# Kernel tuning notes

Measured on AMD Instinct MI355X. Metric: run time of the kernel, lower is better.

The kernel has to match this reference:

```python
import jax, jax.numpy as jnp
import numpy as np

N_GAUSS = 2048
FEAT_DIM = 3
IMG_H, IMG_W = 256, 256
EPS = 1e-4  # args.eps with tiled rasterizer path


def setup_inputs() -> dict:
    key = jax.random.key(0)
    k_xy, k_sc, k_rot, k_feat = jax.random.split(key, 4)
    xy = jax.random.uniform(k_xy, (N_GAUSS, 2), dtype=jnp.float32)  # normalized [0,1) coords
    # scale holds INVERSE std-devs (disable_inverse_scale=False path: scale = 1/init_scale);
    # values 10..50 give Gaussians spanning a few pixels at 256x256.
    scale = jax.random.uniform(k_sc, (N_GAUSS, 2), minval=10.0, maxval=50.0, dtype=jnp.float32)
    rot = jax.random.normal(k_rot, (N_GAUSS, 1), dtype=jnp.float32)
    feat = jax.random.uniform(k_feat, (N_GAUSS, FEAT_DIM), dtype=jnp.float32)
    return {"xy": xy, "scale": scale, "rot": rot, "feat": feat, "topk": 8}


def reference(xy, scale, rot, feat, topk):
    # Pixel centers in normalized coordinates, matching get_grid(h, w) -> (x, y)
    xs = (jnp.arange(IMG_W, dtype=jnp.float32) + 0.5) / IMG_W
    ys = (jnp.arange(IMG_H, dtype=jnp.float32) + 0.5) / IMG_H
    px, py = jnp.meshgrid(xs, ys, indexing="xy")  # each [H, W]
    px = px.reshape(-1)  # [P]
    py = py.reshape(-1)

    dx = px[:, None] - xy[None, :, 0]  # [P, N]
    dy = py[:, None] - xy[None, :, 1]  # [P, N]

    c = jnp.cos(rot[:, 0])  # [N]
    s = jnp.sin(rot[:, 0])
    # Rotate offset into the Gaussian's local frame
    lx = dx * c + dy * s   # [P, N]
    ly = -dx * s + dy * c  # [P, N]

    # Anisotropic Gaussian weight; scale is the inverse std-dev per axis
    w = jnp.exp(-0.5 * ((lx * scale[:, 0]) ** 2 + (ly * scale[:, 1]) ** 2))  # [P, N]

    # Keep top-k Gaussians per pixel, normalize their weights, accumulate features
    tw, ti = jax.lax.top_k(w, topk)        # [P, K]
    tf = feat[ti]                          # [P, K, C]
    alpha = tw / (jnp.sum(tw, axis=-1, keepdims=True) + EPS)  # [P, K]
    img = jnp.einsum("pk,pkc->pc", alpha, tf)                 # [P, C]
    return img.reshape(IMG_H, IMG_W, FEAT_DIM).transpose(2, 0, 1)  # [C, H, W]
```

## Files before the change

### kernel.cpp

```cpp
#include <hip/hip_runtime.h>
#include <math.h>

#define N_GAUSS 2048
#define IMG_H 256
#define IMG_W 256
#define NPIX (IMG_H * IMG_W)
#define EPS 1e-4f

#define TILE 8
#define TILES_X (IMG_W / TILE)
#define NTILES (TILES_X * (IMG_H / TILE))
#define SEG 512
#define SEGCAP 128
#define D_HALF 0.019336f

#define LADDER(T, G)                                                     \
    if ((T) < v7) {                                                      \
        const bool c0 = (T) < v0, c1 = (T) < v1, c2 = (T) < v2;          \
        const bool c3 = (T) < v3, c4 = (T) < v4, c5 = (T) < v5;          \
        const bool c6 = (T) < v6;                                        \
        v7 = c6 ? v6 : (T);            i7 = c6 ? i6 : (G);               \
        v6 = c6 ? (c5 ? v5 : (T)) : v6; i6 = c6 ? (c5 ? i5 : (G)) : i6;  \
        v5 = c5 ? (c4 ? v4 : (T)) : v5; i5 = c5 ? (c4 ? i4 : (G)) : i5;  \
        v4 = c4 ? (c3 ? v3 : (T)) : v4; i4 = c4 ? (c3 ? i3 : (G)) : i4;  \
        v3 = c3 ? (c2 ? v2 : (T)) : v3; i3 = c3 ? (c2 ? i2 : (G)) : i3;  \
        v2 = c2 ? (c1 ? v1 : (T)) : v2; i2 = c2 ? (c1 ? i1 : (G)) : i2;  \
        v1 = c1 ? (c0 ? v0 : (T)) : v1; i1 = c1 ? (c0 ? i0 : (G)) : i1;  \
        v0 = c0 ? (T) : v0;            i0 = c0 ? (G) : i0;               \
    }

#define CE(a, i, j)                                   \
    { float lo_ = fminf(a[i], a[j]);                  \
      float hi_ = fmaxf(a[i], a[j]);                  \
      a[i] = lo_; a[j] = hi_; }

#define SORT8(a)                                      \
    CE(a,0,1) CE(a,2,3) CE(a,4,5) CE(a,6,7)           \
    CE(a,0,2) CE(a,1,3) CE(a,4,6) CE(a,5,7)           \
    CE(a,1,2) CE(a,5,6)                               \
    CE(a,0,4) CE(a,1,5) CE(a,2,6) CE(a,3,7)           \
    CE(a,2,4) CE(a,3,5)                               \
    CE(a,1,2) CE(a,3,4) CE(a,5,6)

__device__ __forceinline__ void top8_butterfly(float (&cur)[8]) {
#pragma unroll
    for (int m = 1; m < 64; m <<= 1) {
        float oth[8];
#pragma unroll
        for (int k = 0; k < 8; ++k) oth[k] = __shfl_xor(cur[k], m, 64);
        float t_[8];
#pragma unroll
        for (int k = 0; k < 8; ++k) t_[k] = fminf(cur[k], oth[7 - k]);
        CE(t_,0,4) CE(t_,1,5) CE(t_,2,6) CE(t_,3,7)
        CE(t_,0,2) CE(t_,1,3) CE(t_,4,6) CE(t_,5,7)
        CE(t_,0,1) CE(t_,2,3) CE(t_,4,5) CE(t_,6,7)
#pragma unroll
        for (int k = 0; k < 8; ++k) cur[k] = t_[k];
    }
}

#define PROC_EXACT(AX, AY, AC, AS, BX, BY, G)                            \
    {                                                                    \
        float dx = __fsub_rn(px, (AX));                                  \
        float dy = __fsub_rn(py, (AY));                                  \
        float lx = __fadd_rn(__fmul_rn(dx, (AC)), __fmul_rn(dy, (AS)));  \
        float ly = __fadd_rn(__fmul_rn(-dx, (AS)), __fmul_rn(dy, (AC))); \
        float aa = __fmul_rn(lx, (BX));                                  \
        float bb = __fmul_rn(ly, (BY));                                  \
        float t2 = __fadd_rn(__fmul_rn(aa, aa), __fmul_rn(bb, bb));      \
        LADDER(t2, (G))                                                  \
    }

__launch_bounds__(256, 4)
__global__ void fused_kernel(const float* __restrict__ xy,
                             const float* __restrict__ scale,
                             const float* __restrict__ rot,
                             const float* __restrict__ feat,
                             float* __restrict__ out) {
    __shared__ float4 qa[4][SEGCAP];
    __shared__ float  qr[4][SEGCAP];
    __shared__ float2 qt[4][SEGCAP];
    __shared__ unsigned short qidx[4][SEG];
    __shared__ float          lt[4][8][64];
    __shared__ unsigned short li[4][8][64];

    const int tid  = threadIdx.x;
    const int lane = tid & 63;
    const int w    = tid >> 6;
    const int tile = blockIdx.x;

    const float cx = (float)((tile & (TILES_X - 1)) * TILE + 4) * (1.0f / IMG_W);
    const float cy = (float)((tile / TILES_X) * TILE + 4) * (1.0f / IMG_H);

    float2 xy_r[8], sc_r[8];
    float  rot_r[8], rlo_r[8];
    float  cur[8];
#pragma unroll
    for (int s = 0; s < 8; ++s) {
        int g = w * SEG + s * 64 + lane;
        xy_r[s]  = ((const float2*)xy)[g];
        sc_r[s]  = ((const float2*)scale)[g];
        rot_r[s] = rot[g];
        float sn, cs2;
        __sincosf(rot_r[s], &sn, &cs2);
        float dx = cx - xy_r[s].x;
        float dy = cy - xy_r[s].y;
        float lx = dx * cs2 + dy * sn;
        float ly = dy * cs2 - dx * sn;
        float a  = lx * sc_r[s].x;
        float b  = ly * sc_r[s].y;
        float rr = sqrtf(a * a + b * b);
        float m  = fmaxf(sc_r[s].x, sc_r[s].y) * D_HALF;
        rlo_r[s] = rr - m;
        cur[s]   = rr + m;
    }

    SORT8(cur)
    top8_butterfly(cur);
    float cut = cur[7];
    cut = cut + 0.01f + 1e-4f * cut;

    unsigned base = 0;
#pragma unroll
    for (int s = 0; s < 8; ++s) {
        bool keep = rlo_r[s] <= cut;
        unsigned long long mask = __ballot(keep);
        if (keep) {
            unsigned pos = base + (unsigned)__popcll(mask & ((1ull << lane) - 1ull));
            qidx[w][pos] = (unsigned short)(w * SEG + s * 64 + lane);
            if (pos < SEGCAP) {
                qa[w][pos] = make_float4(xy_r[s].x, xy_r[s].y, sc_r[s].x, sc_r[s].y);
                qr[w][pos] = rot_r[s];
            }
        }
        base += (unsigned)__popcll(mask);
    }
    const int cnt = (int)base;

    const int pxi = (tile & (TILES_X - 1)) * TILE + (lane & 7);
    const int pyi = (tile / TILES_X) * TILE + (lane >> 3);
    const int p   = pyi * IMG_W + pxi;
    const float px = (pxi + 0.5f) * (1.0f / IMG_W);
    const float py = (pyi + 0.5f) * (1.0f / IMG_H);

    float v0 = INFINITY, v1 = INFINITY, v2 = INFINITY, v3 = INFINITY;
    float v4 = INFINITY, v5 = INFINITY, v6 = INFINITY, v7 = INFINITY;
    int   i0 = 0, i1 = 0, i2 = 0, i3 = 0, i4 = 0, i5 = 0, i6 = 0, i7 = 0;

    const int jcap = cnt < SEGCAP ? cnt : SEGCAP;
    for (int b = 0; b < jcap; b += 64) {
        int t = b + lane;
        if (t < jcap) {
            double sd, cd;
            sincos((double)qr[w][t], &sd, &cd);
            qt[w][t] = make_float2((float)cd, (float)sd);
        }
        int lim = (b + 64 < jcap) ? b + 64 : jcap;
        for (int j = b; j < lim; ++j) {
            float4 a4 = qa[w][j];
            float2 ct = qt[w][j];
            int    g  = (int)qidx[w][j];
            PROC_EXACT(a4.x, a4.y, ct.x, ct.y, a4.z, a4.w, g)
        }
    }
    for (int j = SEGCAP; j < cnt; ++j) {
        int g = (int)qidx[w][j];
        float2 xyg = ((const float2*)xy)[g];
        float2 scg = ((const float2*)scale)[g];
        double sd, cd;
        sincos((double)rot[g], &sd, &cd);
        PROC_EXACT(xyg.x, xyg.y, (float)cd, (float)sd, scg.x, scg.y, g)
    }

    lt[w][0][lane] = v0; li[w][0][lane] = (unsigned short)i0;
    lt[w][1][lane] = v1; li[w][1][lane] = (unsigned short)i1;
    lt[w][2][lane] = v2; li[w][2][lane] = (unsigned short)i2;
    lt[w][3][lane] = v3; li[w][3][lane] = (unsigned short)i3;
    lt[w][4][lane] = v4; li[w][4][lane] = (unsigned short)i4;
    lt[w][5][lane] = v5; li[w][5][lane] = (unsigned short)i5;
    lt[w][6][lane] = v6; li[w][6][lane] = (unsigned short)i6;
    lt[w][7][lane] = v7; li[w][7][lane] = (unsigned short)i7;
    __syncthreads();

    if (w == 0) {
        v0 = INFINITY; v1 = INFINITY; v2 = INFINITY; v3 = INFINITY;
        v4 = INFINITY; v5 = INFINITY; v6 = INFINITY; v7 = INFINITY;
        i0 = 0; i1 = 0; i2 = 0; i3 = 0; i4 = 0; i5 = 0; i6 = 0; i7 = 0;
        for (int c = 0; c < 4; ++c) {
#pragma unroll
            for (int k = 0; k < 8; ++k) {
                float t2 = lt[c][k][lane];
                int   g  = (int)li[c][k][lane];
                LADDER(t2, g)
            }
        }
        float w0 = expf(-0.5f * v0), w1 = expf(-0.5f * v1);
        float w2 = expf(-0.5f * v2), w3 = expf(-0.5f * v3);
        float w4 = expf(-0.5f * v4), w5 = expf(-0.5f * v5);
        float w6 = expf(-0.5f * v6), w7 = expf(-0.5f * v7);
        float sum = w0 + w1 + w2 + w3 + w4 + w5 + w6 + w7;
        float inv = 1.0f / (sum + EPS);

        float oc0 = 0.f, oc1 = 0.f, oc2 = 0.f;
#define ACC(K)                                                  \
        {                                                       \
            float al = w##K * inv;                              \
            const float* f = feat + 3 * i##K;                   \
            oc0 = fmaf(al, f[0], oc0);                          \
            oc1 = fmaf(al, f[1], oc1);                          \
            oc2 = fmaf(al, f[2], oc2);                          \
        }
        ACC(0) ACC(1) ACC(2) ACC(3) ACC(4) ACC(5) ACC(6) ACC(7)
#undef ACC

        out[p]            = oc0;
        out[p + NPIX]     = oc1;
        out[p + 2 * NPIX] = oc2;
    }
}

extern "C" void kernel_launch(void* const* d_in, const int* in_sizes, int n_in,
                              void* d_out, int out_size, void* d_ws, size_t ws_size,
                              hipStream_t stream) {
    const float* xy    = (const float*)d_in[0];
    const float* scale = (const float*)d_in[1];
    const float* rot   = (const float*)d_in[2];
    const float* feat  = (const float*)d_in[3];
    float* out = (float*)d_out;

    fused_kernel<<<NTILES, 256, 0, stream>>>(xy, scale, rot, feat, out);
}
```

Measured before the change: 26.16 us.

## Split gaussians across eight waves per tile and shuffle-broadcast overflow candidates

Doubles the block to 512 threads so each of eight wavefronts handles 256 gaussians instead of 512. This halves the per-wave candidate scan and the serial per-pixel ladder work. Parameters are reloaded from global memory instead of held in registers, and the shared-memory cap shrinks to 64. The overflow path now loads candidates cooperatively and broadcasts them with shuffles instead of serial per-candidate global loads and double sincos. The cost is a longer final merge in wave 0 (eight partial lists instead of four) and higher register pressure under the new launch bounds.

Result: slower. 35.50 us (+35.7%).

```diff
diff --git a/kernel.cpp b/kernel.cpp
--- a/kernel.cpp
+++ b/kernel.cpp
@@ -10,8 +10,9 @@
 #define TILE 8
 #define TILES_X (IMG_W / TILE)
 #define NTILES (TILES_X * (IMG_H / TILE))
-#define SEG 512
-#define SEGCAP 128
+#define NW 8
+#define SEG (N_GAUSS / NW)
+#define CAP 64
 #define D_HALF 0.019336f
 
 #define LADDER(T, G)                                                     \
@@ -34,13 +35,7 @@
       float hi_ = fmaxf(a[i], a[j]);                  \
       a[i] = lo_; a[j] = hi_; }
 
-#define SORT8(a)                                      \
-    CE(a,0,1) CE(a,2,3) CE(a,4,5) CE(a,6,7)           \
-    CE(a,0,2) CE(a,1,3) CE(a,4,6) CE(a,5,7)           \
-    CE(a,1,2) CE(a,5,6)                               \
-    CE(a,0,4) CE(a,1,5) CE(a,2,6) CE(a,3,7)           \
-    CE(a,2,4) CE(a,3,5)                               \
-    CE(a,1,2) CE(a,3,4) CE(a,5,6)
+#define SORT4(a) CE(a,0,1) CE(a,2,3) CE(a,0,2) CE(a,1,3) CE(a,1,2)
 
 __device__ __forceinline__ void top8_butterfly(float (&cur)[8]) {
 #pragma unroll
@@ -71,18 +66,17 @@
         LADDER(t2, (G))                                                  \
     }
 
-__launch_bounds__(256, 4)
+__launch_bounds__(512, 8)
 __global__ void fused_kernel(const float* __restrict__ xy,
                              const float* __restrict__ scale,
                              const float* __restrict__ rot,
                              const float* __restrict__ feat,
                              float* __restrict__ out) {
-    __shared__ float4 qa[4][SEGCAP];
-    __shared__ float  qr[4][SEGCAP];
-    __shared__ float2 qt[4][SEGCAP];
-    __shared__ unsigned short qidx[4][SEG];
-    __shared__ float          lt[4][8][64];
-    __shared__ unsigned short li[4][8][64];
+    __shared__ float4 qa[NW][CAP];
+    __shared__ float2 qt[NW][CAP];
+    __shared__ unsigned short qidx[NW][SEG];
+    __shared__ float          lt[NW][8][64];
+    __shared__ unsigned short li[NW][8][64];
 
     const int tid  = threadIdx.x;
     const int lane = tid & 63;
@@ -92,50 +86,59 @@
     const float cx = (float)((tile & (TILES_X - 1)) * TILE + 4) * (1.0f / IMG_W);
     const float cy = (float)((tile / TILES_X) * TILE + 4) * (1.0f / IMG_H);
 
-    float2 xy_r[8], sc_r[8];
-    float  rot_r[8], rlo_r[8];
-    float  cur[8];
-#pragma unroll
-    for (int s = 0; s < 8; ++s) {
+    float rot_r[4], rlo_r[4], cur[8];
+#pragma unroll
+    for (int s = 0; s < 4; ++s) {
         int g = w * SEG + s * 64 + lane;
-        xy_r[s]  = ((const float2*)xy)[g];
-        sc_r[s]  = ((const float2*)scale)[g];
+        float2 xyg = ((const float2*)xy)[g];
+        float2 scg = ((const float2*)scale)[g];
         rot_r[s] = rot[g];
         float sn, cs2;
         __sincosf(rot_r[s], &sn, &cs2);
-        float dx = cx - xy_r[s].x;
-        float dy = cy - xy_r[s].y;
+        float dx = cx - xyg.x;
+        float dy = cy - xyg.y;
         float lx = dx * cs2 + dy * sn;
         float ly = dy * cs2 - dx * sn;
-        float a  = lx * sc_r[s].x;
-        float b  = ly * sc_r[s].y;
+        float a  = lx * scg.x;
+        float b  = ly * scg.y;
         float rr = sqrtf(a * a + b * b);
-        float m  = fmaxf(sc_r[s].x, sc_r[s].y) * D_HALF;
+        float m  = fmaxf(scg.x, scg.y) * D_HALF;
         rlo_r[s] = rr - m;
         cur[s]   = rr + m;
     }
-
-    SORT8(cur)
+    cur[4] = INFINITY; cur[5] = INFINITY; cur[6] = INFINITY; cur[7] = INFINITY;
+    SORT4(cur)
+
     top8_butterfly(cur);
     float cut = cur[7];
     cut = cut + 0.01f + 1e-4f * cut;
 
     unsigned base = 0;
 #pragma unroll
-    for (int s = 0; s < 8; ++s) {
+    for (int s = 0; s < 4; ++s) {
+        int g = w * SEG + s * 64 + lane;
         bool keep = rlo_r[s] <= cut;
         unsigned long long mask = __ballot(keep);
         if (keep) {
             unsigned pos = base + (unsigned)__popcll(mask & ((1ull << lane) - 1ull));
-            qidx[w][pos] = (unsigned short)(w * SEG + s * 64 + lane);
-            if (pos < SEGCAP) {
-                qa[w][pos] = make_float4(xy_r[s].x, xy_r[s].y, sc_r[s].x, sc_r[s].y);
-                qr[w][pos] = rot_r[s];
+            qidx[w][pos] = (unsigned short)g;
+            if (pos < CAP) {
+                float2 xyg = ((const float2*)xy)[g];
+                float2 scg = ((const float2*)scale)[g];
+                qa[w][pos] = make_float4(xyg.x, xyg.y, scg.x, scg.y);
+                qt[w][pos].x = rot_r[s];
             }
         }
         base += (unsigned)__popcll(mask);
     }
     const int cnt = (int)base;
+
+    const int jcap = cnt < CAP ? cnt : CAP;
+    if (lane < jcap) {
+        double sd, cd;
+        sincos((double)qt[w][lane].x, &sd, &cd);
+        qt[w][lane] = make_float2((float)cd, (float)sd);
+    }
 
     const int pxi = (tile & (TILES_X - 1)) * TILE + (lane & 7);
     const int pyi = (tile / TILES_X) * TILE + (lane >> 3);
@@ -147,29 +150,31 @@
     float v4 = INFINITY, v5 = INFINITY, v6 = INFINITY, v7 = INFINITY;
     int   i0 = 0, i1 = 0, i2 = 0, i3 = 0, i4 = 0, i5 = 0, i6 = 0, i7 = 0;
 
-    const int jcap = cnt < SEGCAP ? cnt : SEGCAP;
-    for (int b = 0; b < jcap; b += 64) {
+    for (int j = 0; j < jcap; ++j) {
+        float4 a4 = qa[w][j];
+        float2 ct = qt[w][j];
+        int    g  = (int)qidx[w][j];
+        PROC_EXACT(a4.x, a4.y, ct.x, ct.y, a4.z, a4.w, g)
+    }
+    for (int b = CAP; b < cnt; b += 64) {
         int t = b + lane;
-        if (t < jcap) {
-            double sd, cd;
-            sincos((double)qr[w][t], &sd, &cd);
-            qt[w][t] = make_float2((float)cd, (float)sd);
-        }
-        int lim = (b + 64 < jcap) ? b + 64 : jcap;
-        for (int j = b; j < lim; ++j) {
-            float4 a4 = qa[w][j];
-            float2 ct = qt[w][j];
-            int    g  = (int)qidx[w][j];
-            PROC_EXACT(a4.x, a4.y, ct.x, ct.y, a4.z, a4.w, g)
-        }
-    }
-    for (int j = SEGCAP; j < cnt; ++j) {
-        int g = (int)qidx[w][j];
-        float2 xyg = ((const float2*)xy)[g];
-        float2 scg = ((const float2*)scale)[g];
+        int gg = (t < cnt) ? (int)qidx[w][t] : 0;
+        float2 xyg = ((const float2*)xy)[gg];
+        float2 scg = ((const float2*)scale)[gg];
         double sd, cd;
-        sincos((double)rot[g], &sd, &cd);
-        PROC_EXACT(xyg.x, xyg.y, (float)cd, (float)sd, scg.x, scg.y, g)
+        sincos((double)rot[gg], &sd, &cd);
+        float cc = (float)cd, ss = (float)sd;
+        int lim = cnt - b; if (lim > 64) lim = 64;
+        for (int j = 0; j < lim; ++j) {
+            float ax = __shfl(xyg.x, j, 64);
+            float ay = __shfl(xyg.y, j, 64);
+            float ac = __shfl(cc,    j, 64);
+            float sn = __shfl(ss,    j, 64);
+            float bx = __shfl(scg.x, j, 64);
+            float by = __shfl(scg.y, j, 64);
+            int   g  = __shfl(gg,    j, 64);
+            PROC_EXACT(ax, ay, ac, sn, bx, by, g)
+        }
     }
 
     lt[w][0][lane] = v0; li[w][0][lane] = (unsigned short)i0;
@@ -186,7 +191,7 @@
         v0 = INFINITY; v1 = INFINITY; v2 = INFINITY; v3 = INFINITY;
         v4 = INFINITY; v5 = INFINITY; v6 = INFINITY; v7 = INFINITY;
         i0 = 0; i1 = 0; i2 = 0; i3 = 0; i4 = 0; i5 = 0; i6 = 0; i7 = 0;
-        for (int c = 0; c < 4; ++c) {
+        for (int c = 0; c < NW; ++c) {
 #pragma unroll
             for (int k = 0; k < 8; ++k) {
                 float t2 = lt[c][k][lane];
@@ -228,5 +233,5 @@
     const float* feat  = (const float*)d_in[3];
     float* out = (float*)d_out;
 
-    fused_kernel<<<NTILES, 256, 0, stream>>>(xy, scale, rot, feat, out);
+    fused_kernel<<<NTILES, 512, 0, stream>>>(xy, scale, rot, feat, out);
 }
```
